# Performance work log

Hardware: AMD Instinct MI355X
Metric: run time of the kernel (lower is better)

## Reference

```python
import jax, jax.numpy as jnp
import numpy as np

H, D, BD = 4, 128, 128   # num_heads, head_dim, bias_dim
QDIM = KDIM = 64
VDIM = 1
N = 512
EPS = 1e-5

def mish(x):
    return x * jnp.tanh(jax.nn.softplus(x))

def layernorm(x, g, b):
    m = jnp.mean(x, axis=-1, keepdims=True)
    v = jnp.var(x, axis=-1, keepdims=True)
    return (x - m) * jax.lax.rsqrt(v + EPS) * g + b

def _xavier(k, shape):
    fan_out, fan_in = shape
    lim = np.sqrt(6.0 / (fan_in + fan_out)).astype(np.float32)
    return jax.random.uniform(k, shape, jnp.float32, -lim, lim)

def setup_inputs() -> dict:
    key = jax.random.key(0)
    ks = jax.random.split(key, 12)
    return {
        "q": jax.random.normal(ks[0], (N, QDIM), jnp.float32),
        "k": jax.random.normal(ks[1], (N, KDIM), jnp.float32),
        "v": jax.random.normal(ks[2], (N, VDIM), jnp.float32),
        "bias": jax.random.uniform(ks[3], (N, N, BD), jnp.float32),
        "Wq": _xavier(ks[4], (H * D, QDIM)), "bq": jnp.zeros((H * D,), jnp.float32),
        "Wk": _xavier(ks[5], (H * D, KDIM)), "bk": jnp.zeros((H * D,), jnp.float32),
        "Wqo": _xavier(ks[6], (QDIM, H * D)), "bqo": jnp.zeros((QDIM,), jnp.float32),
        "Wko": _xavier(ks[7], (KDIM, H * D)), "bko": jnp.zeros((KDIM,), jnp.float32),
        "q_ln_g": jnp.ones((QDIM,), jnp.float32), "q_ln_b": jnp.zeros((QDIM,), jnp.float32),
        "k_ln_g": jnp.ones((KDIM,), jnp.float32), "k_ln_b": jnp.zeros((KDIM,), jnp.float32),
        "Wb": _xavier(ks[8], (H * BD, BD)), "bb_": jnp.zeros((H * BD,), jnp.float32),
        "Wbo": _xavier(ks[9], (BD, H * BD)), "bbo": jnp.zeros((BD,), jnp.float32),
    }

def reference(q, k, v, bias, Wq, bq, Wk, bk, Wqo, bqo, Wko, bko,
              q_ln_g, q_ln_b, k_ln_g, k_ln_b, Wb, bb_, Wbo, bbo):
    Nq, Nk = q.shape[0], k.shape[0]
    # q/k projections -> [N, H, D]
    pq = (q @ Wq.T + bq).reshape(Nq, H, D)
    pk = (k @ Wk.T + bk).reshape(Nk, H, D)
    # distance bias: Linear(BD -> H*BD), per-head L2 norm -> [H, Nq, Nk]
    bias_p = bias @ Wb.T + bb_                                  # [Nq, Nk, H*BD]
    diffs = jnp.linalg.norm(bias_p.reshape(Nq, Nk, H, BD), axis=-1)  # [Nq, Nk, H]
    diffs = jnp.transpose(diffs, (2, 0, 1))                     # [H, Nq, Nk]
    # scaled dot product attention with additive distance bias
    logits = jnp.einsum('qhd,khd->hqk', pq, pk) / np.sqrt(D).astype(np.float32) + diffs
    attn = jax.nn.softmax(logits, axis=-1)                      # [H, Nq, Nk]
    vals = jnp.einsum('hqk,kv->hqv', attn, v)                   # v shared across heads
    # values.permute(1,0,2).reshape(Nq, vdim*H) then mean over last dim
    vals_mean = jnp.mean(jnp.transpose(vals, (1, 0, 2)).reshape(Nq, H * VDIM),
                         axis=-1, keepdims=True)                # [Nq, 1]
    # torch does proj.permute(1,2,0).reshape(N, H*D): (d, h)-major flattening
    pq_flat = jnp.transpose(pq, (0, 2, 1)).reshape(Nq, D * H)
    pk_flat = jnp.transpose(pk, (0, 2, 1)).reshape(Nk, D * H)
    q_new = layernorm(q + mish(pq_flat @ Wqo.T + bqo), q_ln_g, q_ln_b)
    k_new = layernorm(k + mish(pk_flat @ Wko.T + bko), k_ln_g, k_ln_b)
    bias_out = mish(bias_p @ Wbo.T + bbo)                       # [Nq, Nk, BD]
    return (q_new, k_new, vals_mean, bias_out)
```

## Files before the change

kernel.cpp:

```cpp
#include <hip/hip_runtime.h>

#define NN 512
#define MROWS (NN*NN)
#define LDK 136

typedef __attribute__((ext_vector_type(8))) short short8;
typedef __attribute__((ext_vector_type(16))) float floatx16;

__device__ __forceinline__ unsigned short f2bf(float f) {
    union { float f; unsigned u; } x; x.f = f;
    unsigned r = x.u + 0x7fffu + ((x.u >> 16) & 1u);
    return (unsigned short)(r >> 16);
}

__device__ __forceinline__ floatx16 zero16() {
    floatx16 z;
    #pragma unroll
    for (int i = 0; i < 16; ++i) z[i] = 0.f;
    return z;
}

__global__ __launch_bounds__(256) void pre_kernel(
    const float* __restrict__ q, const float* __restrict__ k,
    const float* __restrict__ Wq, const float* __restrict__ bq,
    const float* __restrict__ Wk, const float* __restrict__ bk,
    float* __restrict__ pq, float* __restrict__ pk,
    const float* __restrict__ Wb, const float* __restrict__ Wbo,
    unsigned short* __restrict__ wbf)
{
    int b = blockIdx.x;
    int tid = threadIdx.x;
    if (b >= 1024) {
        int i = (b - 1024) * 256 + tid;
        float v = (i < 65536) ? Wb[i] : Wbo[i - 65536];
        wbf[i] = f2bf(v);
        return;
    }
    __shared__ float xs[64];
    int n = b & 511;
    int is_k = b >> 9;
    const float* x  = is_k ? k  : q;
    const float* W  = is_k ? Wk : Wq;
    const float* bi = is_k ? bk : bq;
    float* out      = is_k ? pk : pq;
    if (tid < 16)
        reinterpret_cast<float4*>(xs)[tid] = reinterpret_cast<const float4*>(x + n*64)[tid];
    __syncthreads();
    #pragma unroll
    for (int jj = 0; jj < 2; ++jj) {
        int j = jj*256 + tid;
        const float4* wr = reinterpret_cast<const float4*>(W + j*64);
        float acc = bi[j];
        #pragma unroll
        for (int c = 0; c < 16; ++c) {
            float4 w4 = wr[c];
            float4 x4 = reinterpret_cast<const float4*>(xs)[c];
            acc += x4.x*w4.x + x4.y*w4.y + x4.z*w4.z + x4.w*w4.w;
        }
        out[n*512 + j] = acc;
    }
}

__global__ __launch_bounds__(256, 4) void bias_kernel(
    const float* __restrict__ bias, const unsigned short* __restrict__ wb_bf,
    const float* __restrict__ bb, const unsigned short* __restrict__ wbo_bf,
    const float* __restrict__ bbo, float* __restrict__ bias_out,
    float* __restrict__ diffs)
{
    __shared__ __align__(16) char smem[34816 + 256];
    unsigned short* lA = (unsigned short*)smem;
    unsigned short* lP = (unsigned short*)(smem + 17408);
    float* sq = (float*)(smem + 34816);
    float* lT = (float*)smem;

    const int tid = threadIdx.x;
    const int w   = tid >> 6;
    const int l   = tid & 63;
    const int l31 = l & 31;
    const int qh  = l >> 5;
    const long row0 = (long)blockIdx.x * 64;

    {
        const float* src = bias + row0 * 128;
        #pragma unroll
        for (int i = 0; i < 4; ++i) {
            int flat = i*2048 + tid*8;
            int r = flat >> 7, c = flat & 127;
            float4 v0 = *reinterpret_cast<const float4*>(src + flat);
            float4 v1 = *reinterpret_cast<const float4*>(src + flat + 4);
            ushort4 o0 = { f2bf(v0.x), f2bf(v0.y), f2bf(v0.z), f2bf(v0.w) };
            ushort4 o1 = { f2bf(v1.x), f2bf(v1.y), f2bf(v1.z), f2bf(v1.w) };
            *reinterpret_cast<ushort4*>(&lA[r*LDK + c])     = o0;
            *reinterpret_cast<ushort4*>(&lA[r*LDK + c + 4]) = o1;
        }
        if (tid < 64) sq[tid] = 0.f;
    }

    floatx16 acc2[2];
    acc2[0] = zero16(); acc2[1] = zero16();

    const unsigned short* wbbase  = wb_bf  + (w*32 + l31)*128 + qh*8;
    const unsigned short* wbobase = wbo_bf + (w*32 + l31)*512 + qh*8;

    __syncthreads();

    for (int h = 0; h < 4; ++h) {
        floatx16 acc1[2];
        acc1[0] = zero16(); acc1[1] = zero16();
        const unsigned short* wa = wbbase + h*16384;
        #pragma unroll
        for (int kk = 0; kk < 8; ++kk) {
            short8 afr = *reinterpret_cast<const short8*>(wa + kk*16);
            short8 b0  = *reinterpret_cast<const short8*>(&lA[(l31)*LDK      + kk*16 + qh*8]);
            short8 b1  = *reinterpret_cast<const short8*>(&lA[(32 + l31)*LDK + kk*16 + qh*8]);
            acc1[0] = __builtin_amdgcn_mfma_f32_32x32x16_bf16(afr, b0, acc1[0], 0, 0, 0);
            acc1[1] = __builtin_amdgcn_mfma_f32_32x32x16_bf16(afr, b1, acc1[1], 0, 0, 0);
        }

        float4 bbq[4];
        #pragma unroll
        for (int s = 0; s < 4; ++s)
            bbq[s] = *reinterpret_cast<const float4*>(bb + h*128 + w*32 + qh*4 + s*8);

        float ssum[2];
        ushort4 pk4[2][4];
        #pragma unroll
        for (int nt = 0; nt < 2; ++nt) {
            float sa = 0.f;
            #pragma unroll
            for (int s = 0; s < 4; ++s) {
                const float* bbp = (const float*)&bbq[s];
                float v0 = acc1[nt][s*4+0] + bbp[0];
                float v1 = acc1[nt][s*4+1] + bbp[1];
                float v2 = acc1[nt][s*4+2] + bbp[2];
                float v3 = acc1[nt][s*4+3] + bbp[3];
                sa += v0*v0 + v1*v1 + v2*v2 + v3*v3;
                pk4[nt][s] = (ushort4){ f2bf(v0), f2bf(v1), f2bf(v2), f2bf(v3) };
            }
            sa += __shfl_xor(sa, 32);
            ssum[nt] = sa;
        }

        __syncthreads();

        #pragma unroll
        for (int nt = 0; nt < 2; ++nt) {
            int m = nt*32 + l31;
            #pragma unroll
            for (int s = 0; s < 4; ++s)
                *reinterpret_cast<ushort4*>(&lP[m*LDK + w*32 + qh*4 + s*8]) = pk4[nt][s];
            if (l < 32) atomicAdd(&sq[m], ssum[nt]);
        }

        __syncthreads();

        if (tid < 64) {
            float s2 = sq[tid];
            diffs[(long)h*MROWS + row0 + tid] = sqrtf(s2);
            sq[tid] = 0.f;
        }

        const unsigned short* wo = wbobase + h*128;
        #pragma unroll
        for (int kk = 0; kk < 8; ++kk) {
            short8 afr = *reinterpret_cast<const short8*>(wo + kk*16);
            short8 b0  = *reinterpret_cast<const short8*>(&lP[(l31)*LDK      + kk*16 + qh*8]);
            short8 b1  = *reinterpret_cast<const short8*>(&lP[(32 + l31)*LDK + kk*16 + qh*8]);
            acc2[0] = __builtin_amdgcn_mfma_f32_32x32x16_bf16(afr, b0, acc2[0], 0, 0, 0);
            acc2[1] = __builtin_amdgcn_mfma_f32_32x32x16_bf16(afr, b1, acc2[1], 0, 0, 0);
        }
    }

    float4 bboq[4];
    #pragma unroll
    for (int s = 0; s < 4; ++s)
        bboq[s] = *reinterpret_cast<const float4*>(bbo + w*32 + qh*4 + s*8);

    float outs[2][16];
    #pragma unroll
    for (int nt = 0; nt < 2; ++nt) {
        #pragma unroll
        for (int s = 0; s < 4; ++s) {
            const float* bp = (const float*)&bboq[s];
            #pragma unroll
            for (int r = 0; r < 4; ++r) {
                float x = acc2[nt][s*4+r] + bp[r];
                float e = __expf(x);
                float u = 1.f + e, u2 = u*u;
                outs[nt][s*4+r] = (x > 15.f) ? x : x * (u2 - 1.f) / (u2 + 1.f);
            }
        }
    }

    __syncthreads();
    #pragma unroll
    for (int nt = 0; nt < 2; ++nt) {
        int m = nt*32 + l31;
        #pragma unroll
        for (int s = 0; s < 4; ++s)
            #pragma unroll
            for (int r = 0; r < 4; ++r)
                lT[m*LDK + w*32 + qh*4 + s*8 + r] = outs[nt][s*4+r];
    }
    __syncthreads();
    #pragma unroll
    for (int i = 0; i < 8; ++i) {
        int flat = i*1024 + tid*4;
        int r = flat >> 7, c = flat & 127;
        *reinterpret_cast<float4*>(bias_out + (row0 + r)*128 + c) =
            *reinterpret_cast<const float4*>(&lT[r*LDK + c]);
    }
}

__global__ __launch_bounds__(256) void qk_kernel(
    const float* __restrict__ pq, const float* __restrict__ pk,
    float* __restrict__ logits)
{
    __shared__ float A[64*128];
    __shared__ float BT[128*64];
    int blk = blockIdx.x;
    int kt = blk & 7, h = (blk >> 3) & 3, qt = blk >> 5;
    int tid = threadIdx.x;

    #pragma unroll
    for (int i = 0; i < 8; ++i) {
        int flat = i*1024 + tid*4;
        int r = flat >> 7, c = flat & 127;
        *reinterpret_cast<float4*>(&A[flat]) =
            *reinterpret_cast<const float4*>(pq + (size_t)(qt*64 + r)*512 + h*128 + c);
    }
    {
        int kk = tid & 63, g = tid >> 6;
        #pragma unroll
        for (int i = 0; i < 8; ++i) {
            int d0 = g*32 + i*4;
            float4 vv = *reinterpret_cast<const float4*>(pk + (size_t)(kt*64 + kk)*512 + h*128 + d0);
            BT[(d0+0)*64 + kk] = vv.x;
            BT[(d0+1)*64 + kk] = vv.y;
            BT[(d0+2)*64 + kk] = vv.z;
            BT[(d0+3)*64 + kk] = vv.w;
        }
    }
    __syncthreads();

    int qg = tid >> 4, kg = tid & 15;
    int qs = qg*4, ks = kg*4;
    float acc[4][4] = {};
    for (int d = 0; d < 128; d += 4) {
        float a_[4][4], b_[4][4];
        #pragma unroll
        for (int i = 0; i < 4; ++i) {
            float4 av = *reinterpret_cast<const float4*>(&A[(qs+i)*128 + d]);
            a_[i][0] = av.x; a_[i][1] = av.y; a_[i][2] = av.z; a_[i][3] = av.w;
        }
        #pragma unroll
        for (int dd = 0; dd < 4; ++dd) {
            float4 bv = *reinterpret_cast<const float4*>(&BT[(d+dd)*64 + ks]);
            b_[dd][0] = bv.x; b_[dd][1] = bv.y; b_[dd][2] = bv.z; b_[dd][3] = bv.w;
        }
        #pragma unroll
        for (int i = 0; i < 4; ++i)
            #pragma unroll
            for (int j = 0; j < 4; ++j)
                acc[i][j] += a_[i][0]*b_[0][j] + a_[i][1]*b_[1][j]
                           + a_[i][2]*b_[2][j] + a_[i][3]*b_[3][j];
    }

    const float scale = 0.088388347648318447f;
    #pragma unroll
    for (int i = 0; i < 4; ++i) {
        size_t off = (size_t)h*MROWS + (size_t)(qt*64 + qs + i)*512 + kt*64 + ks;
        float4* p = reinterpret_cast<float4*>(logits + off);
        float4 dv = *p;
        dv.x = fmaf(acc[i][0], scale, dv.x);
        dv.y = fmaf(acc[i][1], scale, dv.y);
        dv.z = fmaf(acc[i][2], scale, dv.z);
        dv.w = fmaf(acc[i][3], scale, dv.w);
        *p = dv;
    }
}

__global__ __launch_bounds__(256) void attnval_kernel(
    const float* __restrict__ logits, const float* __restrict__ v,
    float* __restrict__ vmean)
{
    __shared__ float red[32];
    int qrow = blockIdx.x, tid = threadIdx.x;
    int wid = tid >> 6;
    float vsum = 0.f;
    float v0 = v[tid], v1 = v[tid + 256];
    for (int h = 0; h < 4; ++h) {
        const float* lr = logits + (size_t)h*MROWS + (size_t)qrow*512;
        float l0 = lr[tid], l1 = lr[tid + 256];
        float m = fmaxf(l0, l1);
        #pragma unroll
        for (int o = 1; o < 64; o <<= 1) m = fmaxf(m, __shfl_xor(m, o));
        if ((tid & 63) == 0) red[wid] = m;
        __syncthreads();
        m = fmaxf(fmaxf(red[0], red[1]), fmaxf(red[2], red[3]));
        float e0 = __expf(l0 - m), e1 = __expf(l1 - m);
        float s = e0 + e1;
        float sv = e0*v0 + e1*v1;
        #pragma unroll
        for (int o = 1; o < 64; o <<= 1) { s += __shfl_xor(s, o); sv += __shfl_xor(sv, o); }
        __syncthreads();
        if ((tid & 63) == 0) { red[8 + wid] = s; red[16 + wid] = sv; }
        __syncthreads();
        float S  = red[8]  + red[9]  + red[10] + red[11];
        float SV = red[16] + red[17] + red[18] + red[19];
        vsum += SV / S;
        __syncthreads();
    }
    if (tid == 0) vmean[qrow] = vsum * 0.25f;
}

__global__ __launch_bounds__(256) void qkout_kernel(
    const float* __restrict__ p, const float* __restrict__ x,
    const float* __restrict__ W, const float* __restrict__ bo,
    const float* __restrict__ g, const float* __restrict__ be,
    float* __restrict__ out)
{
    __shared__ float pr[512];
    __shared__ float red[256];
    int n = blockIdx.x, tid = threadIdx.x;
    if (tid < 128)
        reinterpret_cast<float4*>(pr)[tid] = reinterpret_cast<const float4*>(p + (size_t)n*512)[tid];
    __syncthreads();
    int o = tid >> 2, part = tid & 3;
    const float4* wr = reinterpret_cast<const float4*>(W + o*512 + part*128);
    float acc = 0.f;
    #pragma unroll
    for (int c = 0; c < 32; ++c) {
        float4 w4 = wr[c];
        int base = part*32 + c;
        acc += pr[base]*w4.x + pr[128 + base]*w4.y + pr[256 + base]*w4.z + pr[384 + base]*w4.w;
    }
    red[tid] = acc;
    __syncthreads();
    if (tid < 64) {
        float s = red[tid*4] + red[tid*4+1] + red[tid*4+2] + red[tid*4+3] + bo[tid];
        float e = __expf(s);
        float u = 1.f + e, u2 = u*u;
        float msh = (s > 15.f) ? s : s * (u2 - 1.f) / (u2 + 1.f);
        float val = x[n*64 + tid] + msh;
        float m = val, m2 = val*val;
        #pragma unroll
        for (int off = 1; off < 64; off <<= 1) { m += __shfl_xor(m, off); m2 += __shfl_xor(m2, off); }
        m *= (1.f/64.f); m2 *= (1.f/64.f);
        float var = m2 - m*m;
        out[n*64 + tid] = (val - m) * rsqrtf(var + 1e-5f) * g[tid] + be[tid];
    }
}

extern "C" void kernel_launch(void* const* d_in, const int* in_sizes, int n_in,
                              void* d_out, int out_size, void* d_ws, size_t ws_size,
                              hipStream_t stream) {
    const float* q    = (const float*)d_in[0];
    const float* k    = (const float*)d_in[1];
    const float* v    = (const float*)d_in[2];
    const float* bias = (const float*)d_in[3];
    const float* Wq   = (const float*)d_in[4];
    const float* bq   = (const float*)d_in[5];
    const float* Wk   = (const float*)d_in[6];
    const float* bk   = (const float*)d_in[7];
    const float* Wqo  = (const float*)d_in[8];
    const float* bqo  = (const float*)d_in[9];
    const float* Wko  = (const float*)d_in[10];
    const float* bko  = (const float*)d_in[11];
    const float* qlg  = (const float*)d_in[12];
    const float* qlb  = (const float*)d_in[13];
    const float* klg  = (const float*)d_in[14];
    const float* klb  = (const float*)d_in[15];
    const float* Wb   = (const float*)d_in[16];
    const float* bb   = (const float*)d_in[17];
    const float* Wbo  = (const float*)d_in[18];
    const float* bbo  = (const float*)d_in[19];

    float* out = (float*)d_out;
    float* ws  = (float*)d_ws;
    float* diffs = ws;
    float* pq    = ws + 4*MROWS;
    float* pk    = pq + MROWS;
    unsigned short* wbf = (unsigned short*)(pk + MROWS);

    float* q_new = out;
    float* k_new = out + 32768;
    float* vmean = out + 65536;
    float* b_out = out + 66048;

    pre_kernel<<<dim3(1536), dim3(256), 0, stream>>>(q, k, Wq, bq, Wk, bk, pq, pk, Wb, Wbo, wbf);
    bias_kernel<<<dim3(4096), dim3(256), 0, stream>>>(bias, wbf, bb, wbf + 65536, bbo, b_out, diffs);
    qk_kernel<<<dim3(256), dim3(256), 0, stream>>>(pq, pk, diffs);
    attnval_kernel<<<dim3(512), dim3(256), 0, stream>>>(diffs, v, vmean);
    qkout_kernel<<<dim3(512), dim3(256), 0, stream>>>(pq, q, Wqo, bqo, qlg, qlb, q_new);
    qkout_kernel<<<dim3(512), dim3(256), 0, stream>>>(pk, k, Wko, bko, klg, klb, k_new);
}
```

Before: 447.4 us.

## Keep bias projection intermediates in registers and give each wave its own rows

The bias kernel is restructured so each wave owns 32 rows of a 128-row tile. The projected bias slice stays in registers and is passed to the second MFMA via a cross-half-wave shuffle, instead of round-tripping through LDS with block barriers and atomics. The L2-norm reduction is done per wave and written directly, and the mish output is stored straight from registers without an LDS transpose. Each wave now loads all weight tiles itself, raising global/L2 weight traffic and register pressure (launch bound lowered to 3 blocks/SIMD). In exchange it removes most syncthreads and LDS traffic.

```diff
diff --git a/kernel.cpp b/kernel.cpp
--- a/kernel.cpp
+++ b/kernel.cpp
@@ -61,29 +61,26 @@
     }
 }
 
-__global__ __launch_bounds__(256, 4) void bias_kernel(
+__global__ __launch_bounds__(256, 3) void bias_kernel(
     const float* __restrict__ bias, const unsigned short* __restrict__ wb_bf,
     const float* __restrict__ bb, const unsigned short* __restrict__ wbo_bf,
     const float* __restrict__ bbo, float* __restrict__ bias_out,
     float* __restrict__ diffs)
 {
-    __shared__ __align__(16) char smem[34816 + 256];
-    unsigned short* lA = (unsigned short*)smem;
-    unsigned short* lP = (unsigned short*)(smem + 17408);
-    float* sq = (float*)(smem + 34816);
-    float* lT = (float*)smem;
+    __shared__ __align__(16) unsigned short lA[128 * LDK];
 
     const int tid = threadIdx.x;
     const int w   = tid >> 6;
     const int l   = tid & 63;
     const int l31 = l & 31;
     const int qh  = l >> 5;
-    const long row0 = (long)blockIdx.x * 64;
+    const long row0 = (long)blockIdx.x * 128;
+    const int wm = w * 32;
 
     {
         const float* src = bias + row0 * 128;
         #pragma unroll
-        for (int i = 0; i < 4; ++i) {
+        for (int i = 0; i < 8; ++i) {
             int flat = i*2048 + tid*8;
             int r = flat >> 7, c = flat & 127;
             float4 v0 = *reinterpret_cast<const float4*>(src + flat);
@@ -93,122 +90,86 @@
             *reinterpret_cast<ushort4*>(&lA[r*LDK + c])     = o0;
             *reinterpret_cast<ushort4*>(&lA[r*LDK + c + 4]) = o1;
         }
-        if (tid < 64) sq[tid] = 0.f;
-    }
-
-    floatx16 acc2[2];
-    acc2[0] = zero16(); acc2[1] = zero16();
-
-    const unsigned short* wbbase  = wb_bf  + (w*32 + l31)*128 + qh*8;
-    const unsigned short* wbobase = wbo_bf + (w*32 + l31)*512 + qh*8;
-
-    __syncthreads();
-
+    }
+    __syncthreads();
+
+    short8 bfr[8];
+    #pragma unroll
+    for (int kk = 0; kk < 8; ++kk)
+        bfr[kk] = *reinterpret_cast<const short8*>(&lA[(wm + l31)*LDK + kk*16 + qh*8]);
+
+    floatx16 acc2[4];
+    #pragma unroll
+    for (int u = 0; u < 4; ++u) acc2[u] = zero16();
+
+    const unsigned short* wbA  = wb_bf  + l31*128 + qh*8;
+    const unsigned short* wboA = wbo_bf + l31*512 + qh*8;
+
+    #pragma unroll 1
     for (int h = 0; h < 4; ++h) {
-        floatx16 acc1[2];
-        acc1[0] = zero16(); acc1[1] = zero16();
-        const unsigned short* wa = wbbase + h*16384;
-        #pragma unroll
-        for (int kk = 0; kk < 8; ++kk) {
-            short8 afr = *reinterpret_cast<const short8*>(wa + kk*16);
-            short8 b0  = *reinterpret_cast<const short8*>(&lA[(l31)*LDK      + kk*16 + qh*8]);
-            short8 b1  = *reinterpret_cast<const short8*>(&lA[(32 + l31)*LDK + kk*16 + qh*8]);
-            acc1[0] = __builtin_amdgcn_mfma_f32_32x32x16_bf16(afr, b0, acc1[0], 0, 0, 0);
-            acc1[1] = __builtin_amdgcn_mfma_f32_32x32x16_bf16(afr, b1, acc1[1], 0, 0, 0);
-        }
-
-        float4 bbq[4];
-        #pragma unroll
-        for (int s = 0; s < 4; ++s)
-            bbq[s] = *reinterpret_cast<const float4*>(bb + h*128 + w*32 + qh*4 + s*8);
-
-        float ssum[2];
-        ushort4 pk4[2][4];
-        #pragma unroll
-        for (int nt = 0; nt < 2; ++nt) {
-            float sa = 0.f;
-            #pragma unroll
-            for (int s = 0; s < 4; ++s) {
-                const float* bbp = (const float*)&bbq[s];
-                float v0 = acc1[nt][s*4+0] + bbp[0];
-                float v1 = acc1[nt][s*4+1] + bbp[1];
-                float v2 = acc1[nt][s*4+2] + bbp[2];
-                float v3 = acc1[nt][s*4+3] + bbp[3];
-                sa += v0*v0 + v1*v1 + v2*v2 + v3*v3;
-                pk4[nt][s] = (ushort4){ f2bf(v0), f2bf(v1), f2bf(v2), f2bf(v3) };
+        float dsum = 0.f;
+        #pragma unroll
+        for (int t = 0; t < 4; ++t) {
+            floatx16 acc1 = zero16();
+            #pragma unroll
+            for (int kk = 0; kk < 8; ++kk) {
+                short8 afr = *reinterpret_cast<const short8*>(wbA + h*16384 + t*4096 + kk*16);
+                acc1 = __builtin_amdgcn_mfma_f32_32x32x16_bf16(afr, bfr[kk], acc1, 0, 0, 0);
             }
-            sa += __shfl_xor(sa, 32);
-            ssum[nt] = sa;
-        }
-
-        __syncthreads();
-
-        #pragma unroll
-        for (int nt = 0; nt < 2; ++nt) {
-            int m = nt*32 + l31;
-            #pragma unroll
-            for (int s = 0; s < 4; ++s)
-                *reinterpret_cast<ushort4*>(&lP[m*LDK + w*32 + qh*4 + s*8]) = pk4[nt][s];
-            if (l < 32) atomicAdd(&sq[m], ssum[nt]);
-        }
-
-        __syncthreads();
-
-        if (tid < 64) {
-            float s2 = sq[tid];
-            diffs[(long)h*MROWS + row0 + tid] = sqrtf(s2);
-            sq[tid] = 0.f;
-        }
-
-        const unsigned short* wo = wbobase + h*128;
-        #pragma unroll
-        for (int kk = 0; kk < 8; ++kk) {
-            short8 afr = *reinterpret_cast<const short8*>(wo + kk*16);
-            short8 b0  = *reinterpret_cast<const short8*>(&lP[(l31)*LDK      + kk*16 + qh*8]);
-            short8 b1  = *reinterpret_cast<const short8*>(&lP[(32 + l31)*LDK + kk*16 + qh*8]);
-            acc2[0] = __builtin_amdgcn_mfma_f32_32x32x16_bf16(afr, b0, acc2[0], 0, 0, 0);
-            acc2[1] = __builtin_amdgcn_mfma_f32_32x32x16_bf16(afr, b1, acc2[1], 0, 0, 0);
-        }
-    }
-
-    float4 bboq[4];
-    #pragma unroll
-    for (int s = 0; s < 4; ++s)
-        bboq[s] = *reinterpret_cast<const float4*>(bbo + w*32 + qh*4 + s*8);
-
-    float outs[2][16];
-    #pragma unroll
-    for (int nt = 0; nt < 2; ++nt) {
-        #pragma unroll
-        for (int s = 0; s < 4; ++s) {
-            const float* bp = (const float*)&bboq[s];
-            #pragma unroll
-            for (int r = 0; r < 4; ++r) {
-                float x = acc2[nt][s*4+r] + bp[r];
+            unsigned packed[8];
+            #pragma unroll
+            for (int j = 0; j < 4; ++j) {
+                float4 b4 = *reinterpret_cast<const float4*>(bb + h*128 + t*32 + j*8 + qh*4);
+                float p0 = acc1[4*j+0] + b4.x;
+                float p1 = acc1[4*j+1] + b4.y;
+                float p2 = acc1[4*j+2] + b4.z;
+                float p3 = acc1[4*j+3] + b4.w;
+                dsum += p0*p0 + p1*p1 + p2*p2 + p3*p3;
+                packed[2*j]   = (unsigned)f2bf(p0) | ((unsigned)f2bf(p1) << 16);
+                packed[2*j+1] = (unsigned)f2bf(p2) | ((unsigned)f2bf(p3) << 16);
+            }
+            #pragma unroll
+            for (int sg = 0; sg < 2; ++sg) {
+                unsigned sA = qh ? packed[4*sg]     : packed[4*sg+2];
+                unsigned sB = qh ? packed[4*sg+1]   : packed[4*sg+3];
+                unsigned rA = (unsigned)__shfl_xor((int)sA, 32);
+                unsigned rB = (unsigned)__shfl_xor((int)sB, 32);
+                union { unsigned u[4]; short8 s; } pf;
+                pf.u[0] = qh ? rA : packed[4*sg];
+                pf.u[1] = qh ? rB : packed[4*sg+1];
+                pf.u[2] = qh ? packed[4*sg+2] : rA;
+                pf.u[3] = qh ? packed[4*sg+3] : rB;
+                #pragma unroll
+                for (int u = 0; u < 4; ++u) {
+                    short8 afr = *reinterpret_cast<const short8*>(
+                        wboA + u*16384 + h*128 + t*32 + sg*16);
+                    acc2[u] = __builtin_amdgcn_mfma_f32_32x32x16_bf16(afr, pf.s, acc2[u], 0, 0, 0);
+                }
+            }
+        }
+        dsum += __shfl_xor(dsum, 32);
+        if (qh == 0)
+            diffs[(long)h*MROWS + row0 + wm + l31] = sqrtf(dsum);
+    }
+
+    const long orow = (row0 + wm + l31) * 128;
+    #pragma unroll
+    for (int u = 0; u < 4; ++u) {
+        #pragma unroll
+        for (int j = 0; j < 4; ++j) {
+            float4 b4 = *reinterpret_cast<const float4*>(bbo + u*32 + j*8 + qh*4);
+            float4 o;
+            float* op = (float*)&o;
+            const float* bp = (const float*)&b4;
+            #pragma unroll
+            for (int b = 0; b < 4; ++b) {
+                float x = acc2[u][4*j+b] + bp[b];
                 float e = __expf(x);
-                float u = 1.f + e, u2 = u*u;
-                outs[nt][s*4+r] = (x > 15.f) ? x : x * (u2 - 1.f) / (u2 + 1.f);
+                float un = 1.f + e, u2 = un*un;
+                op[b] = (x > 15.f) ? x : x * (u2 - 1.f) / (u2 + 1.f);
             }
-        }
-    }
-
-    __syncthreads();
-    #pragma unroll
-    for (int nt = 0; nt < 2; ++nt) {
-        int m = nt*32 + l31;
-        #pragma unroll
-        for (int s = 0; s < 4; ++s)
-            #pragma unroll
-            for (int r = 0; r < 4; ++r)
-                lT[m*LDK + w*32 + qh*4 + s*8 + r] = outs[nt][s*4+r];
-    }
-    __syncthreads();
-    #pragma unroll
-    for (int i = 0; i < 8; ++i) {
-        int flat = i*1024 + tid*4;
-        int r = flat >> 7, c = flat & 127;
-        *reinterpret_cast<float4*>(bias_out + (row0 + r)*128 + c) =
-            *reinterpret_cast<const float4*>(&lT[r*LDK + c]);
+            *reinterpret_cast<float4*>(bias_out + orow + u*32 + j*8 + qh*4) = o;
+        }
     }
 }
 
@@ -389,7 +350,7 @@
     float* b_out = out + 66048;
 
     pre_kernel<<<dim3(1536), dim3(256), 0, stream>>>(q, k, Wq, bq, Wk, bk, pq, pk, Wb, Wbo, wbf);
-    bias_kernel<<<dim3(4096), dim3(256), 0, stream>>>(bias, wbf, bb, wbf + 65536, bbo, b_out, diffs);
+    bias_kernel<<<dim3(2048), dim3(256), 0, stream>>>(bias, wbf, bb, wbf + 65536, bbo, b_out, diffs);
     qk_kernel<<<dim3(256), dim3(256), 0, stream>>>(pq, pk, diffs);
     attnval_kernel<<<dim3(512), dim3(256), 0, stream>>>(diffs, v, vmean);
     qkout_kernel<<<dim3(512), dim3(256), 0, stream>>>(pq, q, Wqo, bqo, qlg, qlb, q_new);
```

Result: slower. 659.6 us (+47.4%).
